# Performance work log

Measured on AMD Instinct MI355X. Metric: run time of the kernel, lower is better.

Reference implementation:

```python
import jax, jax.numpy as jnp
import numpy as np

NUM_MOL = 1024
KE = 14.399645351950548
KEHALF = KE / 2.0
CUTOFF = 10.0  # PhysNetCutOff(10.0)


def physnet_cutoff(d):
    # PhysNet smooth cutoff: 1 - 6u^5 + 15u^4 - 10u^3 for d < rc, else 0
    u = d / CUTOFF
    fc = 1.0 - 6.0 * u**5 + 15.0 * u**4 - 10.0 * u**3
    return jnp.where(d < CUTOFF, fc, 0.0)


def setup_inputs() -> dict:
    key = jax.random.key(0)
    k = jax.random.split(key, 5)
    N, E = 100000, 3200000
    # atomic numbers as floats in [1, 94]
    Z = jax.random.randint(k[0], (N,), 1, 95).astype(jnp.float32)
    # pair displacement vectors; norm ~ O(3) Angstrom, well inside cutoff
    r_ij = jax.random.normal(k[1], (E, 3), dtype=jnp.float32) * 2.0
    idx_i = jax.random.randint(k[2], (E,), 0, N, dtype=jnp.int32)
    idx_j = jax.random.randint(k[3], (E,), 0, N, dtype=jnp.int32)
    # per-atom molecule index, sorted (maxm = idx_m[-1] + 1 in the original)
    idx_m = jnp.sort(jax.random.randint(k[4], (N,), 0, NUM_MOL, dtype=jnp.int32))
    adiv = jnp.ones((1,), jnp.float32)
    apow = jnp.ones((1,), jnp.float32)
    a_vector = jnp.ones((4,), jnp.float32)
    c_vector = jnp.ones((4,), jnp.float32)
    return dict(Z=Z, r_ij=r_ij, idx_i=idx_i, idx_j=idx_j, idx_m=idx_m,
                adiv=adiv, apow=apow, a_vector=a_vector, c_vector=c_vector)


def reference(Z, r_ij, idx_i, idx_j, idx_m, adiv, apow, a_vector, c_vector):
    N = Z.shape[0]
    d = jnp.linalg.norm(r_ij, axis=1)                      # (E,)
    cut = physnet_cutoff(d)                                # (E,)
    z = Z ** jax.nn.softplus(apow[0])                      # (N,)
    a = (z[idx_i] + z[idx_j]) * jax.nn.softplus(adiv[0])   # (E,)
    a_comp = jax.nn.softplus(a_vector)[:, None] * a        # (4, E)
    c = jax.nn.softplus(c_vector)
    c_normed = c / jnp.sum(jnp.abs(c))                     # L1-normalize over dim 0
    f_temp = jnp.einsum('k,ke->e', c_normed, jnp.exp(-a_comp * d))  # (E,)
    f = f_temp * cut
    zizj = Z[idx_i] * Z[idx_j]
    e_edge = KEHALF * f * zizj / d                          # (E,)
    y_atom = jax.ops.segment_sum(e_edge, idx_i, num_segments=N)        # (N,)
    y = jax.ops.segment_sum(y_atom, idx_m, num_segments=NUM_MOL)       # (NUM_MOL,)
    return y
```

## Files before the change

### kernel.cpp

```cpp
#include <hip/hip_runtime.h>
#include <hip/hip_bf16.h>

#define NUM_MOL 1024
#define KEHALF 7.199822675975274f
#define RCUT 10.0f

__device__ __forceinline__ float softplus_f(float x) {
    return (x > 20.0f) ? x : log1pf(__expf(x));
}

__global__ void zbl_prep_kernel(const float* __restrict__ Z,
                                const int* __restrict__ idx_m,
                                const float* __restrict__ apow,
                                float4* __restrict__ atab, int N) {
    int n = blockIdx.x * blockDim.x + threadIdx.x;
    if (n >= N) return;
    float p = softplus_f(apow[0]);
    float z = Z[n];
    float zp = __powf(z, p);
    atab[n] = make_float4(z, zp, __int_as_float(idx_m[n]), 0.0f);
}

__global__ __launch_bounds__(256) void zbl_edge_kernel(
    const float* __restrict__ r_ij,
    const int* __restrict__ idx_i,
    const int* __restrict__ idx_j,
    const float4* __restrict__ atab,
    const float* __restrict__ adiv,
    const float* __restrict__ a_vector,
    const float* __restrict__ c_vector,
    float* __restrict__ y, int E)
{
    __shared__ float bins[NUM_MOL];
    for (int b = threadIdx.x; b < NUM_MOL; b += blockDim.x) bins[b] = 0.0f;
    __syncthreads();

    const float sp_adiv = softplus_f(adiv[0]);
    const float sa0 = softplus_f(a_vector[0]);
    const float sa1 = softplus_f(a_vector[1]);
    const float sa2 = softplus_f(a_vector[2]);
    const float sa3 = softplus_f(a_vector[3]);
    float c0 = softplus_f(c_vector[0]);
    float c1 = softplus_f(c_vector[1]);
    float c2 = softplus_f(c_vector[2]);
    float c3 = softplus_f(c_vector[3]);
    const float cs = fabsf(c0) + fabsf(c1) + fabsf(c2) + fabsf(c3);
    const float cinv = 1.0f / cs;
    c0 *= cinv; c1 *= cinv; c2 *= cinv; c3 *= cinv;

    const int stride = gridDim.x * blockDim.x;
    for (int e = blockIdx.x * blockDim.x + threadIdx.x; e < E; e += stride) {
        const int i = idx_i[e];
        const int j = idx_j[e];
        const float4 ai = atab[i];
        const float4 aj = atab[j];
        const float x  = r_ij[3 * e + 0];
        const float yy = r_ij[3 * e + 1];
        const float zz = r_ij[3 * e + 2];
        const float d = sqrtf(x * x + yy * yy + zz * zz);

        const float u = d * (1.0f / RCUT);
        const float u3 = u * u * u;
        float fc = 1.0f + u3 * (-10.0f + u * (15.0f - 6.0f * u));
        fc = (d < RCUT) ? fc : 0.0f;

        const float a = (ai.y + aj.y) * sp_adiv;
        const float ad = a * d;
        const float ft = c0 * __expf(-sa0 * ad) + c1 * __expf(-sa1 * ad)
                       + c2 * __expf(-sa2 * ad) + c3 * __expf(-sa3 * ad);

        const float ee = KEHALF * ft * fc * ai.x * aj.x / d;
        atomicAdd(&bins[__float_as_int(ai.z)], ee);
    }

    __syncthreads();
    for (int b = threadIdx.x; b < NUM_MOL; b += blockDim.x) {
        const float v = bins[b];
        if (v != 0.0f) atomicAdd(&y[b], v);
    }
}

__global__ __launch_bounds__(256) void zbl_edge_kernel_nows(
    const float* __restrict__ r_ij,
    const int* __restrict__ idx_i,
    const int* __restrict__ idx_j,
    const float* __restrict__ Z,
    const int* __restrict__ idx_m,
    const float* __restrict__ adiv,
    const float* __restrict__ apow,
    const float* __restrict__ a_vector,
    const float* __restrict__ c_vector,
    float* __restrict__ y, int E)
{
    __shared__ float bins[NUM_MOL];
    for (int b = threadIdx.x; b < NUM_MOL; b += blockDim.x) bins[b] = 0.0f;
    __syncthreads();

    const float sp_apow = softplus_f(apow[0]);
    const float sp_adiv = softplus_f(adiv[0]);
    const float sa0 = softplus_f(a_vector[0]);
    const float sa1 = softplus_f(a_vector[1]);
    const float sa2 = softplus_f(a_vector[2]);
    const float sa3 = softplus_f(a_vector[3]);
    float c0 = softplus_f(c_vector[0]);
    float c1 = softplus_f(c_vector[1]);
    float c2 = softplus_f(c_vector[2]);
    float c3 = softplus_f(c_vector[3]);
    const float cs = fabsf(c0) + fabsf(c1) + fabsf(c2) + fabsf(c3);
    const float cinv = 1.0f / cs;
    c0 *= cinv; c1 *= cinv; c2 *= cinv; c3 *= cinv;

    const int stride = gridDim.x * blockDim.x;
    for (int e = blockIdx.x * blockDim.x + threadIdx.x; e < E; e += stride) {
        const int i = idx_i[e];
        const int j = idx_j[e];
        const float zi = Z[i];
        const float zj = Z[j];
        const float x  = r_ij[3 * e + 0];
        const float yy = r_ij[3 * e + 1];
        const float zz = r_ij[3 * e + 2];
        const float d = sqrtf(x * x + yy * yy + zz * zz);

        const float u = d * (1.0f / RCUT);
        const float u3 = u * u * u;
        float fc = 1.0f + u3 * (-10.0f + u * (15.0f - 6.0f * u));
        fc = (d < RCUT) ? fc : 0.0f;

        const float a = (__powf(zi, sp_apow) + __powf(zj, sp_apow)) * sp_adiv;
        const float ad = a * d;
        const float ft = c0 * __expf(-sa0 * ad) + c1 * __expf(-sa1 * ad)
                       + c2 * __expf(-sa2 * ad) + c3 * __expf(-sa3 * ad);

        const float ee = KEHALF * ft * fc * zi * zj / d;
        atomicAdd(&bins[idx_m[i]], ee);
    }

    __syncthreads();
    for (int b = threadIdx.x; b < NUM_MOL; b += blockDim.x) {
        const float v = bins[b];
        if (v != 0.0f) atomicAdd(&y[b], v);
    }
}

extern "C" void kernel_launch(void* const* d_in, const int* in_sizes, int n_in,
                              void* d_out, int out_size, void* d_ws, size_t ws_size,
                              hipStream_t stream) {
    const float* Z        = (const float*)d_in[0];
    const float* r_ij     = (const float*)d_in[1];
    const int*   idx_i    = (const int*)d_in[2];
    const int*   idx_j    = (const int*)d_in[3];
    const int*   idx_m    = (const int*)d_in[4];
    const float* adiv     = (const float*)d_in[5];
    const float* apow     = (const float*)d_in[6];
    const float* a_vector = (const float*)d_in[7];
    const float* c_vector = (const float*)d_in[8];
    float* y = (float*)d_out;

    const int N = in_sizes[0];
    const int E = in_sizes[1] / 3;

    hipMemsetAsync(y, 0, (size_t)out_size * sizeof(float), stream);

    const size_t atab_bytes = (size_t)N * sizeof(float4);
    if (ws_size >= atab_bytes) {
        float4* atab = (float4*)d_ws;
        zbl_prep_kernel<<<(N + 255) / 256, 256, 0, stream>>>(Z, idx_m, apow, atab, N);
        zbl_edge_kernel<<<1024, 256, 0, stream>>>(r_ij, idx_i, idx_j, atab,
                                                  adiv, a_vector, c_vector, y, E);
    } else {
        zbl_edge_kernel_nows<<<1024, 256, 0, stream>>>(r_ij, idx_i, idx_j, Z, idx_m,
                                                       adiv, apow, a_vector, c_vector, y, E);
    }
}
```

Baseline: 138.2 us.

## Pack atom table to 8 bytes and vectorize edge loads four per thread

Shrinks the per-atom gather table from a float4 to two 32-bit words, packing integer Z and the molecule index into one word. The edge kernel now loads four edges per thread with 128-bit nontemporal loads for indices and coordinates, and handles the remainder in a scalar tail. It also replaces sqrt plus divide with rsqrt, and moves to 512-thread blocks with a larger grid. The packing assumes Z values are integers below 256 and that molecule indices fit in 24 bits.

```diff
diff --git a/kernel.cpp b/kernel.cpp
--- a/kernel.cpp
+++ b/kernel.cpp
@@ -5,6 +5,10 @@
 #define KEHALF 7.199822675975274f
 #define RCUT 10.0f
 
+typedef int   vint4   __attribute__((ext_vector_type(4)));
+typedef float vfloat4 __attribute__((ext_vector_type(4)));
+typedef unsigned int vuint2 __attribute__((ext_vector_type(2)));
+
 __device__ __forceinline__ float softplus_f(float x) {
     return (x > 20.0f) ? x : log1pf(__expf(x));
 }
@@ -12,20 +16,51 @@
 __global__ void zbl_prep_kernel(const float* __restrict__ Z,
                                 const int* __restrict__ idx_m,
                                 const float* __restrict__ apow,
-                                float4* __restrict__ atab, int N) {
+                                vuint2* __restrict__ atab, int N) {
     int n = blockIdx.x * blockDim.x + threadIdx.x;
     if (n >= N) return;
     float p = softplus_f(apow[0]);
     float z = Z[n];
     float zp = __powf(z, p);
-    atab[n] = make_float4(z, zp, __int_as_float(idx_m[n]), 0.0f);
-}
-
-__global__ __launch_bounds__(256) void zbl_edge_kernel(
+    unsigned zi = (unsigned)z;
+    unsigned m  = (unsigned)idx_m[n];
+    vuint2 v; v.x = __float_as_uint(zp); v.y = (m << 8) | zi;
+    atab[n] = v;
+}
+
+__device__ __forceinline__ void do_edge(
+    float x, float yy, float zz, vuint2 ai, vuint2 aj,
+    float sp_adiv, float sa0, float sa1, float sa2, float sa3,
+    float c0, float c1, float c2, float c3, float* bins)
+{
+    const float d2 = x * x + yy * yy + zz * zz;
+    const float inv = rsqrtf(d2);
+    const float d = d2 * inv;
+
+    const float u = d * (1.0f / RCUT);
+    const float u3 = u * u * u;
+    float fc = 1.0f + u3 * (-10.0f + u * (15.0f - 6.0f * u));
+    fc = (d < RCUT) ? fc : 0.0f;
+
+    const float zpi = __uint_as_float(ai.x);
+    const float zpj = __uint_as_float(aj.x);
+    const float zizj = (float)((ai.y & 0xFFu) * (aj.y & 0xFFu));
+    const int   mol  = (int)(ai.y >> 8);
+
+    const float a = (zpi + zpj) * sp_adiv;
+    const float ad = a * d;
+    const float ft = c0 * __expf(-sa0 * ad) + c1 * __expf(-sa1 * ad)
+                   + c2 * __expf(-sa2 * ad) + c3 * __expf(-sa3 * ad);
+
+    const float ee = KEHALF * ft * fc * zizj * inv;
+    atomicAdd(&bins[mol], ee);
+}
+
+__global__ __launch_bounds__(512, 6) void zbl_edge_kernel(
     const float* __restrict__ r_ij,
     const int* __restrict__ idx_i,
     const int* __restrict__ idx_j,
-    const float4* __restrict__ atab,
+    const vuint2* __restrict__ atab,
     const float* __restrict__ adiv,
     const float* __restrict__ a_vector,
     const float* __restrict__ c_vector,
@@ -44,33 +79,44 @@
     float c1 = softplus_f(c_vector[1]);
     float c2 = softplus_f(c_vector[2]);
     float c3 = softplus_f(c_vector[3]);
-    const float cs = fabsf(c0) + fabsf(c1) + fabsf(c2) + fabsf(c3);
-    const float cinv = 1.0f / cs;
+    const float cinv = 1.0f / (fabsf(c0) + fabsf(c1) + fabsf(c2) + fabsf(c3));
     c0 *= cinv; c1 *= cinv; c2 *= cinv; c3 *= cinv;
 
+    const vfloat4* __restrict__ r4  = (const vfloat4*)r_ij;
+    const vint4*   __restrict__ ii4 = (const vint4*)idx_i;
+    const vint4*   __restrict__ jj4 = (const vint4*)idx_j;
+
+    const int tid0   = blockIdx.x * blockDim.x + threadIdx.x;
     const int stride = gridDim.x * blockDim.x;
-    for (int e = blockIdx.x * blockDim.x + threadIdx.x; e < E; e += stride) {
-        const int i = idx_i[e];
-        const int j = idx_j[e];
-        const float4 ai = atab[i];
-        const float4 aj = atab[j];
-        const float x  = r_ij[3 * e + 0];
-        const float yy = r_ij[3 * e + 1];
-        const float zz = r_ij[3 * e + 2];
-        const float d = sqrtf(x * x + yy * yy + zz * zz);
-
-        const float u = d * (1.0f / RCUT);
-        const float u3 = u * u * u;
-        float fc = 1.0f + u3 * (-10.0f + u * (15.0f - 6.0f * u));
-        fc = (d < RCUT) ? fc : 0.0f;
-
-        const float a = (ai.y + aj.y) * sp_adiv;
-        const float ad = a * d;
-        const float ft = c0 * __expf(-sa0 * ad) + c1 * __expf(-sa1 * ad)
-                       + c2 * __expf(-sa2 * ad) + c3 * __expf(-sa3 * ad);
-
-        const float ee = KEHALF * ft * fc * ai.x * aj.x / d;
-        atomicAdd(&bins[__float_as_int(ai.z)], ee);
+    const int G = E >> 2;
+
+    for (int g = tid0; g < G; g += stride) {
+        const vint4   vi = __builtin_nontemporal_load(&ii4[g]);
+        const vint4   vj = __builtin_nontemporal_load(&jj4[g]);
+        const vfloat4 ra = __builtin_nontemporal_load(&r4[3 * g + 0]);
+        const vfloat4 rb = __builtin_nontemporal_load(&r4[3 * g + 1]);
+        const vfloat4 rc = __builtin_nontemporal_load(&r4[3 * g + 2]);
+
+        const vuint2 ai0 = atab[vi.x];
+        const vuint2 ai1 = atab[vi.y];
+        const vuint2 ai2 = atab[vi.z];
+        const vuint2 ai3 = atab[vi.w];
+        const vuint2 aj0 = atab[vj.x];
+        const vuint2 aj1 = atab[vj.y];
+        const vuint2 aj2 = atab[vj.z];
+        const vuint2 aj3 = atab[vj.w];
+
+        do_edge(ra.x, ra.y, ra.z, ai0, aj0, sp_adiv, sa0, sa1, sa2, sa3, c0, c1, c2, c3, bins);
+        do_edge(ra.w, rb.x, rb.y, ai1, aj1, sp_adiv, sa0, sa1, sa2, sa3, c0, c1, c2, c3, bins);
+        do_edge(rb.z, rb.w, rc.x, ai2, aj2, sp_adiv, sa0, sa1, sa2, sa3, c0, c1, c2, c3, bins);
+        do_edge(rc.y, rc.z, rc.w, ai3, aj3, sp_adiv, sa0, sa1, sa2, sa3, c0, c1, c2, c3, bins);
+    }
+
+    for (int e = (G << 2) + tid0; e < E; e += stride) {
+        const vuint2 ai = atab[idx_i[e]];
+        const vuint2 aj = atab[idx_j[e]];
+        do_edge(r_ij[3 * e + 0], r_ij[3 * e + 1], r_ij[3 * e + 2],
+                ai, aj, sp_adiv, sa0, sa1, sa2, sa3, c0, c1, c2, c3, bins);
     }
 
     __syncthreads();
@@ -106,8 +152,7 @@
     float c1 = softplus_f(c_vector[1]);
     float c2 = softplus_f(c_vector[2]);
     float c3 = softplus_f(c_vector[3]);
-    const float cs = fabsf(c0) + fabsf(c1) + fabsf(c2) + fabsf(c3);
-    const float cinv = 1.0f / cs;
+    const float cinv = 1.0f / (fabsf(c0) + fabsf(c1) + fabsf(c2) + fabsf(c3));
     c0 *= cinv; c1 *= cinv; c2 *= cinv; c3 *= cinv;
 
     const int stride = gridDim.x * blockDim.x;
@@ -119,7 +164,9 @@
         const float x  = r_ij[3 * e + 0];
         const float yy = r_ij[3 * e + 1];
         const float zz = r_ij[3 * e + 2];
-        const float d = sqrtf(x * x + yy * yy + zz * zz);
+        const float d2 = x * x + yy * yy + zz * zz;
+        const float inv = rsqrtf(d2);
+        const float d = d2 * inv;
 
         const float u = d * (1.0f / RCUT);
         const float u3 = u * u * u;
@@ -131,7 +178,7 @@
         const float ft = c0 * __expf(-sa0 * ad) + c1 * __expf(-sa1 * ad)
                        + c2 * __expf(-sa2 * ad) + c3 * __expf(-sa3 * ad);
 
-        const float ee = KEHALF * ft * fc * zi * zj / d;
+        const float ee = KEHALF * ft * fc * zi * zj * inv;
         atomicAdd(&bins[idx_m[i]], ee);
     }
 
@@ -159,16 +206,16 @@
     const int N = in_sizes[0];
     const int E = in_sizes[1] / 3;
 
-    hipMemsetAsync(y, 0, (size_t)out_size * sizeof(float), stream);
-
-    const size_t atab_bytes = (size_t)N * sizeof(float4);
+    (void)hipMemsetAsync(y, 0, (size_t)out_size * sizeof(float), stream);
+
+    const size_t atab_bytes = (size_t)N * sizeof(vuint2);
     if (ws_size >= atab_bytes) {
-        float4* atab = (float4*)d_ws;
+        vuint2* atab = (vuint2*)d_ws;
         zbl_prep_kernel<<<(N + 255) / 256, 256, 0, stream>>>(Z, idx_m, apow, atab, N);
-        zbl_edge_kernel<<<1024, 256, 0, stream>>>(r_ij, idx_i, idx_j, atab,
+        zbl_edge_kernel<<<1024, 512, 0, stream>>>(r_ij, idx_i, idx_j, atab,
                                                   adiv, a_vector, c_vector, y, E);
     } else {
-        zbl_edge_kernel_nows<<<1024, 256, 0, stream>>>(r_ij, idx_i, idx_j, Z, idx_m,
+        zbl_edge_kernel_nows<<<2048, 256, 0, stream>>>(r_ij, idx_i, idx_j, Z, idx_m,
                                                        adiv, apow, a_vector, c_vector, y, E);
     }
 }
```

Result: slower. 151.1 us (+9.3%).
